# Optimization experiments

Hardware: AMD Instinct MI355X
Metric: run time of the kernel (lower is better)

## Reference

```python
import jax, jax.numpy as jnp
import numpy as np

TAIL = 3.0            # tail bound B of the unconstrained RQS
MIN_W = 1e-3
MIN_H = 1e-3
MIN_D = 1e-3
K = 8                 # number of spline bins


def conv1d(x, w, b):
    # x: [B, Cin, L], w: [Cout, Cin, k] -> [B, Cout, L] (SAME padding)
    y = jax.lax.conv_general_dilated(x, w, (1,), 'SAME',
                                     dimension_numbers=('NCH', 'OIH', 'NCH'))
    return y + b[None, :, None]


def pixelcnn(c, x, w0, b0, wh, bh, w_out, b_out):
    # conditioner: maps (c, x) -> per-channel spline params (W, H, D)
    h = jnp.concatenate([c, x], axis=1)
    h = jax.nn.relu(conv1d(h, w0, b0))
    for j in range(wh.shape[0]):
        h = jax.nn.relu(conv1d(h, wh[j], bh[j]))
    p = conv1d(h, w_out, b_out)        # [B, (3K-1)*C, L]
    p = p.mean(axis=-1)                # global pool over positions
    Bsz, C = x.shape[0], x.shape[1]
    p = p.reshape(Bsz, C, 3 * K - 1)
    return p[..., :K], p[..., K:2 * K], p[..., 2 * K:]


def _gather(p, idx):
    # p: [B, C, Kp], idx: [B, C, L] -> [B, C, L]
    return jnp.take_along_axis(p[:, :, None, :], idx[..., None], axis=-1)[..., 0]


def rqs_inverse(y, Wp, Hp, Dp):
    # Vectorized unconstrained rational-quadratic spline (inverse pass),
    # replacing the torch per-position Python loop; params broadcast over L.
    Kb = Wp.shape[-1]
    widths = MIN_W + (1 - MIN_W * Kb) * jax.nn.softmax(Wp, -1)
    cw = jnp.concatenate([jnp.zeros_like(widths[..., :1]), jnp.cumsum(widths, -1)], -1)
    cw = 2 * TAIL * cw - TAIL                      # knot x-positions [B,C,K+1]
    widths = cw[..., 1:] - cw[..., :-1]
    heights = MIN_H + (1 - MIN_H * Kb) * jax.nn.softmax(Hp, -1)
    ch = jnp.concatenate([jnp.zeros_like(heights[..., :1]), jnp.cumsum(heights, -1)], -1)
    ch = 2 * TAIL * ch - TAIL                      # knot y-positions [B,C,K+1]
    heights = ch[..., 1:] - ch[..., :-1]
    d_int = MIN_D + jax.nn.softplus(Dp)            # interior derivatives [B,C,K-1]
    ones = jnp.ones_like(d_int[..., :1])
    derivs = jnp.concatenate([ones, d_int, ones], -1)   # boundary derivs = 1

    inside = jnp.abs(y) <= TAIL                    # identity tails outside
    yc = jnp.clip(y, -TAIL, TAIL)
    # bin search over K+1 knots (broadcast compare, K is small)
    idx = jnp.clip(jnp.sum((yc[..., None] >= ch[:, :, None, :]), -1) - 1, 0, Kb - 1)

    in_cw = _gather(cw, idx); in_w = _gather(widths, idx)
    in_ch = _gather(ch, idx); in_h = _gather(heights, idx)
    dk = _gather(derivs, idx); dk1 = _gather(derivs, idx + 1)

    s = in_h / in_w
    dy = yc - in_ch
    t1 = dk + dk1 - 2 * s
    a = in_h * (s - dk) + dy * t1
    b = in_h * dk - dy * t1
    cq = -s * dy
    disc = jnp.maximum(b * b - 4 * a * cq, 0.0)
    root = (2 * cq) / (-b - jnp.sqrt(disc))        # xi in [0,1]
    out = root * in_w + in_cw
    denom = s + t1 * root * (1 - root)
    dnum = s * s * (dk1 * root * root + 2 * s * root * (1 - root) + dk * (1 - root) ** 2)
    ld = -(jnp.log(dnum) - 2 * jnp.log(denom))     # inverse logabsdet
    return jnp.where(inside, out, y), jnp.where(inside, ld, jnp.zeros_like(ld))


def flow_forward(c, noise, w0, b0, wh, bh, w_out, b_out):
    x = noise                                      # torch draws fresh N(0,1) of z.shape
    L = x.shape[-1]
    log_det = jnp.zeros((x.shape[0], 1), x.dtype)
    T = w0.shape[0]
    for t in range(T):                             # small fixed number of flow steps
        Wp, Hp, Dp = pixelcnn(c, x, w0[t], b0[t], wh[t], bh[t], w_out[t], b_out[t])
        x, ld = rqs_inverse(x, Wp, Hp, Dp)         # all L positions at once
        # torch: sum_i (sum over channels of ld_i) / L
        log_det = log_det + ld.sum(axis=(1, 2))[:, None] / L
    return x, log_det


def setup_inputs() -> dict:
    key = jax.random.key(0)
    ks = jax.random.split(key, 8)
    B, C_IN, C_OUT, L, T, HID = 128, 16, 8, 8192, 2, 32
    P = 3 * K - 1
    return {
        'z': jax.random.normal(ks[0], (B, C_OUT, L), jnp.float32),
        'c': jax.random.normal(ks[1], (B, C_IN, L), jnp.float32),
        'noise': jax.random.normal(ks[2], (B, C_OUT, L), jnp.float32),
        'w0': 0.1 * jax.random.normal(ks[3], (T, HID, C_IN + C_OUT, 3), jnp.float32),
        'b0': jnp.zeros((T, HID), jnp.float32),
        'wh': 0.1 * jax.random.normal(ks[4], (T, 3, HID, HID, 3), jnp.float32),
        'bh': jnp.zeros((T, 3, HID), jnp.float32),
        'w_out': 0.1 * jax.random.normal(ks[5], (T, P * C_OUT, HID, 1), jnp.float32),
        'b_out': jnp.zeros((T, P * C_OUT), jnp.float32),
    }


def reference(z, c, noise, w0, b0, wh, bh, w_out, b_out):
    del z  # torch forward ignores z's values; it only uses z.shape for the noise draw
    return flow_forward(c, noise, w0, b0, wh, bh, w_out, b_out)
```

## Files before the change

kernel.cpp:

```cpp
#include <hip/hip_runtime.h>
#include <hip/hip_bf16.h>

#define BATCH 128
#define CCOND 16
#define CX    8
#define CIN0  24
#define HID   32
#define LLEN  8192
#define NSTEP 2
#define PDIM  23
#define POUT  184
#define PSTR  48

#define WPW   48
#define SROWS 56
#define RSTR  40
#define LWORDS (SROWS * RSTR)
#define GRIDX 43

typedef __bf16 bf16x8 __attribute__((ext_vector_type(8)));
typedef __bf16 bf16x4 __attribute__((ext_vector_type(4)));
typedef float  f32x4  __attribute__((ext_vector_type(4)));

#define WAVE_SYNC() asm volatile("s_waitcnt lgkmcnt(0)" ::: "memory")

template<int CTRL>
__device__ __forceinline__ float dpp_movf(float v) {
    return __int_as_float(
        __builtin_amdgcn_mov_dpp(__float_as_int(v), CTRL, 0xF, 0xF, true));
}
#define RROR1 0x121
#define RROR2 0x122
#define RROR4 0x124
#define RROR8 0x128

__device__ __forceinline__ unsigned short f2bf(float f) {
    unsigned u = __float_as_uint(f);
    return (unsigned short)((u + 0x7FFFu + ((u >> 16) & 1u)) >> 16);
}

__global__ void zero_kernel(float* __restrict__ ws, float* __restrict__ logdet) {
    int i = blockIdx.x * 256 + threadIdx.x;
    ws[i] = 0.f;
    if (i < BATCH) logdet[i] = 0.f;
}

__global__ void repack_frag_kernel(const float* __restrict__ w0,
                                   const float* __restrict__ wh,
                                   unsigned short* __restrict__ wf) {
    int i = blockIdx.x * 256 + threadIdx.x;
    int j = i & 7, lane = (i >> 3) & 63, q = i >> 9;
    int mt = q & 1; q >>= 1;
    int s = q % 3;  q /= 3;
    int l = q & 3, t = q >> 2;
    int m = mt * 16 + (lane & 15);
    int ci = (lane >> 4) * 8 + j;
    float v;
    if (l == 0)
        v = (ci < CIN0) ? w0[((t * HID + m) * CIN0 + ci) * 3 + s] : 0.f;
    else
        v = wh[(((t * 3 + (l - 1)) * HID + m) * HID + ci) * 3 + s];
    wf[i] = f2bf(v);
}

template<int NTL, int LAST, bool EDGE>
__device__ __forceinline__ void wconv_layer(
        const __bf16* __restrict__ bin, __bf16* __restrict__ bout,
        const unsigned short* __restrict__ wl, const float* __restrict__ bp,
        const int (&starts)[NTL], int gb, int lane, float* __restrict__ vs) {
    const int prow = lane & 15, grp = lane >> 4;
    const int ci0 = grp * 8, co0 = grp * 4;

    bf16x8 af[3][2];
    #pragma unroll
    for (int s = 0; s < 3; ++s)
        #pragma unroll
        for (int mt = 0; mt < 2; ++mt)
            af[s][mt] = *reinterpret_cast<const bf16x8*>(
                wl + ((s * 2 + mt) << 9) + (lane << 3));
    f32x4 bias0 = *reinterpret_cast<const f32x4*>(bp + co0);
    f32x4 bias1 = *reinterpret_cast<const f32x4*>(bp + 16 + co0);

    bf16x8 bfr[NTL][3];
    #pragma unroll
    for (int t = 0; t < NTL; ++t) {
        const int o = starts[t] + prow;
        #pragma unroll
        for (int tap = 0; tap < 3; ++tap)
            bfr[t][tap] = *reinterpret_cast<const bf16x8*>(
                &bin[(o + tap - 1) * RSTR + ci0]);
    }
    __builtin_amdgcn_sched_barrier(0);

    #pragma unroll
    for (int t = 0; t < NTL; ++t) {
        const int o = starts[t] + prow;
        f32x4 a0 = bias0, a1 = bias1;
        a0 = __builtin_amdgcn_mfma_f32_16x16x32_bf16(af[0][0], bfr[t][0], a0, 0, 0, 0);
        a1 = __builtin_amdgcn_mfma_f32_16x16x32_bf16(af[0][1], bfr[t][0], a1, 0, 0, 0);
        a0 = __builtin_amdgcn_mfma_f32_16x16x32_bf16(af[1][0], bfr[t][1], a0, 0, 0, 0);
        a1 = __builtin_amdgcn_mfma_f32_16x16x32_bf16(af[1][1], bfr[t][1], a1, 0, 0, 0);
        a0 = __builtin_amdgcn_mfma_f32_16x16x32_bf16(af[2][0], bfr[t][2], a0, 0, 0, 0);
        a1 = __builtin_amdgcn_mfma_f32_16x16x32_bf16(af[2][1], bfr[t][2], a1, 0, 0, 0);
        bool ok = true;
        if (EDGE) ok = (unsigned)(gb - 4 + o) < (unsigned)LLEN;
        #pragma unroll
        for (int r = 0; r < 4; ++r) {
            a0[r] = fmaxf(a0[r], 0.f);
            a1[r] = fmaxf(a1[r], 0.f);
            if (EDGE) { a0[r] = ok ? a0[r] : 0.f; a1[r] = ok ? a1[r] : 0.f; }
        }
        if (!LAST) {
            bf16x4 p0, p1;
            #pragma unroll
            for (int r = 0; r < 4; ++r) { p0[r] = (__bf16)a0[r]; p1[r] = (__bf16)a1[r]; }
            *reinterpret_cast<bf16x4*>(&bout[o * RSTR + co0]) = p0;
            *reinterpret_cast<bf16x4*>(&bout[o * RSTR + 16 + co0]) = p1;
        } else {
            #pragma unroll
            for (int r = 0; r < 4; ++r) { vs[r] += a0[r]; vs[4 + r] += a1[r]; }
        }
    }
}

template<bool EDGE>
__device__ __forceinline__ void conv_body(
        const float* __restrict__ cin, const float* __restrict__ xin,
        const unsigned short* __restrict__ wf,
        const float* __restrict__ b0p, const float* __restrict__ bhp,
        __bf16* __restrict__ bufA, __bf16* __restrict__ bufB,
        int b, int gb, int lane, float* __restrict__ vs) {
    if (lane < SROWS) {
        const int p = lane;
        int g = gb - 4 + p;
        int gc = g;
        bool ok = true;
        if (EDGE) { gc = min(max(g, 0), LLEN - 1); ok = (g == gc); }
        const float* cbp = cin + (size_t)b * CCOND * LLEN + gc;
        const float* xbp = xin + (size_t)b * CX * LLEN + gc;
        float v[CIN0];
        #pragma unroll
        for (int ch = 0; ch < CCOND; ++ch) v[ch] = cbp[(size_t)ch * LLEN];
        #pragma unroll
        for (int ch = 0; ch < CX; ++ch) v[CCOND + ch] = xbp[(size_t)ch * LLEN];
        if (EDGE) {
            #pragma unroll
            for (int ch = 0; ch < CIN0; ++ch) v[ch] = ok ? v[ch] : 0.f;
        }
        bf16x8 pk0, pk1, pk2;
        #pragma unroll
        for (int j = 0; j < 8; ++j) {
            pk0[j] = (__bf16)v[j];
            pk1[j] = (__bf16)v[8 + j];
            pk2[j] = (__bf16)v[16 + j];
        }
        *reinterpret_cast<bf16x8*>(&bufA[p * RSTR])      = pk0;
        *reinterpret_cast<bf16x8*>(&bufA[p * RSTR + 8])  = pk1;
        *reinterpret_cast<bf16x8*>(&bufA[p * RSTR + 16]) = pk2;
        *reinterpret_cast<uint4*>(&bufA[p * RSTR + 24])  = make_uint4(0, 0, 0, 0);
    }
    WAVE_SYNC();

    const int s0[4] = {1, 17, 33, 39};
    const int s1[4] = {2, 18, 34, 38};
    const int s2[4] = {3, 19, 35, 37};
    const int s3[3] = {4, 20, 36};
    wconv_layer<4, 0, EDGE>(bufA, bufB, wf,        b0p,      s0, gb, lane, vs);
    WAVE_SYNC();
    wconv_layer<4, 0, EDGE>(bufB, bufA, wf + 3072, bhp,      s1, gb, lane, vs);
    WAVE_SYNC();
    wconv_layer<4, 0, EDGE>(bufA, bufB, wf + 6144, bhp + 32, s2, gb, lane, vs);
    WAVE_SYNC();
    wconv_layer<3, 1, EDGE>(bufB, bufA, wf + 9216, bhp + 64, s3, gb, lane, vs);
}

__global__ __launch_bounds__(256, 4) void conv_kernel(
        const float* __restrict__ cin,
        const float* __restrict__ xin,
        const unsigned short* __restrict__ wf,
        const float* __restrict__ b0p,
        const float* __restrict__ bhp,
        float* __restrict__ hbar) {
    __shared__ __align__(16) __bf16 lds[4][2][LWORDS];
    __shared__ float psum[4][HID];

    const int tid = threadIdx.x;
    const int lane = tid & 63, wv = tid >> 6;
    const int b = blockIdx.y;
    const int gb = blockIdx.x * (4 * WPW) + wv * WPW;
    const int prow = lane & 15, grp = lane >> 4;

    __bf16* bufA = &lds[wv][0][0];
    __bf16* bufB = &lds[wv][1][0];

    float vs[8] = {0.f, 0.f, 0.f, 0.f, 0.f, 0.f, 0.f, 0.f};
    const bool edge = (gb < 4) || (gb + SROWS - 4 > LLEN);
    if (edge)
        conv_body<true >(cin, xin, wf, b0p, bhp, bufA, bufB, b, gb, lane, vs);
    else
        conv_body<false>(cin, xin, wf, b0p, bhp, bufA, bufB, b, gb, lane, vs);

    #pragma unroll
    for (int r = 0; r < 8; ++r) {
        vs[r] += dpp_movf<RROR8>(vs[r]);
        vs[r] += dpp_movf<RROR4>(vs[r]);
        vs[r] += dpp_movf<RROR2>(vs[r]);
        vs[r] += dpp_movf<RROR1>(vs[r]);
    }
    const int co0 = grp * 4;
    if (prow == 0) {
        #pragma unroll
        for (int r = 0; r < 4; ++r) {
            psum[wv][co0 + r] = vs[r];
            psum[wv][16 + co0 + r] = vs[4 + r];
        }
    }
    __syncthreads();
    if (tid < HID) {
        float s = psum[0][tid] + psum[1][tid] + psum[2][tid] + psum[3][tid];
        atomicAdd(&hbar[b * HID + tid], s);
    }
}

__device__ __forceinline__ float softplusf(float v) {
    return fmaxf(v, 0.f) + log1pf(expf(-fabsf(v)));
}

__global__ __launch_bounds__(256) void params_kernel(
        const float* __restrict__ hbar,
        const float* __restrict__ w_out,
        const float* __restrict__ b_out,
        float* __restrict__ params) {
    __shared__ float wsh[POUT][HID + 1];
    __shared__ float hsh[32][HID];
    const int tid = threadIdx.x;
    const float invL = 1.0f / (float)LLEN;
    for (int i = tid; i < POUT * HID; i += 256)
        wsh[i >> 5][i & 31] = w_out[i];
    for (int i = tid; i < 32 * HID; i += 256)
        hsh[i >> 5][i & 31] = hbar[blockIdx.x * 32 * HID + i] * invL;
    __syncthreads();

    int tg = blockIdx.x * 256 + tid;
    int bl = tid >> 3, c = tid & 7;

    float p[PDIM];
    #pragma unroll
    for (int j = 0; j < PDIM; j++) {
        int cp = c * PDIM + j;
        float acc = b_out[cp];
        #pragma unroll
        for (int h = 0; h < HID; h++) acc = fmaf(wsh[cp][h], hsh[bl][h], acc);
        p[j] = acc;
    }

    float* out = params + (size_t)tg * PSTR;

    {
        float mx = p[0];
        #pragma unroll
        for (int k = 1; k < 8; k++) mx = fmaxf(mx, p[k]);
        float e[8], se = 0.f;
        #pragma unroll
        for (int k = 0; k < 8; k++) { e[k] = expf(p[k] - mx); se += e[k]; }
        float inv = 1.f / se, cum = 0.f;
        float cw[9]; cw[0] = -3.f;
        #pragma unroll
        for (int k = 0; k < 8; k++) {
            float wk = 1e-3f + (1.f - 8e-3f) * (e[k] * inv);
            cum += wk;
            cw[k + 1] = 6.f * cum - 3.f;
        }
        #pragma unroll
        for (int k = 0; k < 9; k++) out[k] = cw[k];
        #pragma unroll
        for (int k = 0; k < 8; k++) out[18 + k] = cw[k + 1] - cw[k];
    }
    {
        float mx = p[8];
        #pragma unroll
        for (int k = 1; k < 8; k++) mx = fmaxf(mx, p[8 + k]);
        float e[8], se = 0.f;
        #pragma unroll
        for (int k = 0; k < 8; k++) { e[k] = expf(p[8 + k] - mx); se += e[k]; }
        float inv = 1.f / se, cum = 0.f;
        float ch[9]; ch[0] = -3.f;
        #pragma unroll
        for (int k = 0; k < 8; k++) {
            float hk = 1e-3f + (1.f - 8e-3f) * (e[k] * inv);
            cum += hk;
            ch[k + 1] = 6.f * cum - 3.f;
        }
        #pragma unroll
        for (int k = 0; k < 9; k++) out[9 + k] = ch[k];
        #pragma unroll
        for (int k = 0; k < 8; k++) out[26 + k] = ch[k + 1] - ch[k];
    }
    out[34] = 1.f;
    #pragma unroll
    for (int k = 0; k < 7; k++) out[35 + k] = 1e-3f + softplusf(p[16 + k]);
    out[42] = 1.f;
}

__device__ __forceinline__ void rqs_elem(
        const float* cw, const float* chv, const float* wd,
        const float* hg, const float* dv,
        float y, float& ov, float& ldsum) {
    bool inside = fabsf(y) <= 3.0f;
    float yc = fminf(fmaxf(y, -3.f), 3.f);

    float icw = cw[0], iw = wd[0], ich = chv[0], ih = hg[0];
    float dk = dv[0], dk1 = dv[1];
    #pragma unroll
    for (int k = 1; k < 8; k++) {
        bool c = yc >= chv[k];
        icw = c ? cw[k]  : icw;
        iw  = c ? wd[k]  : iw;
        ich = c ? chv[k] : ich;
        ih  = c ? hg[k]  : ih;
        dk  = c ? dv[k]  : dk;
        dk1 = c ? dv[k + 1] : dk1;
    }
    float s  = ih * __builtin_amdgcn_rcpf(iw);
    float dy = yc - ich;
    float t1 = dk + dk1 - 2.f * s;
    float a  = ih * (s - dk) + dy * t1;
    float bq = ih * dk - dy * t1;
    float cq = -s * dy;
    float disc = fmaxf(bq * bq - 4.f * a * cq, 0.f);
    float den  = -bq - __builtin_amdgcn_sqrtf(disc);
    float root = (2.f * cq) * __builtin_amdgcn_rcpf(den);
    float om = 1.f - root;
    float outv  = fmaf(root, iw, icw);
    float denom = fmaf(t1 * root, om, s);
    float dnum  = s * s * (dk1 * root * root + 2.f * s * root * om + dk * om * om);
    float ld = (2.f * __builtin_amdgcn_logf(denom) - __builtin_amdgcn_logf(dnum))
               * 0.69314718055994531f;
    ov = inside ? outv : y;
    ldsum += inside ? ld : 0.f;
}

__global__ __launch_bounds__(256) void rqs_kernel(const float* __restrict__ params,
                                                  const float* __restrict__ xin,
                                                  float* __restrict__ xout,
                                                  float* __restrict__ logdet) {
    const int bc = blockIdx.y;
    const float* __restrict__ pp = params + (size_t)bc * PSTR;
    float cw[9], chv[9], wd[8], hg[8], dv[9];
    #pragma unroll
    for (int k = 0; k < 9; k++) cw[k] = pp[k];
    #pragma unroll
    for (int k = 0; k < 9; k++) chv[k] = pp[9 + k];
    #pragma unroll
    for (int k = 0; k < 8; k++) wd[k] = pp[18 + k];
    #pragma unroll
    for (int k = 0; k < 8; k++) hg[k] = pp[26 + k];
    #pragma unroll
    for (int k = 0; k < 9; k++) dv[k] = pp[34 + k];

    const int tid = threadIdx.x;
    size_t base = (size_t)bc * LLEN + (size_t)blockIdx.x * 4096 + (size_t)tid * 4;
    float4 y4[4];
    #pragma unroll
    for (int q = 0; q < 4; ++q)
        y4[q] = *reinterpret_cast<const float4*>(xin + base + q * 1024);

    float ldsum = 0.f;
    float4 o4[4];
    #pragma unroll
    for (int q = 0; q < 4; ++q) {
        rqs_elem(cw, chv, wd, hg, dv, y4[q].x, o4[q].x, ldsum);
        rqs_elem(cw, chv, wd, hg, dv, y4[q].y, o4[q].y, ldsum);
        rqs_elem(cw, chv, wd, hg, dv, y4[q].z, o4[q].z, ldsum);
        rqs_elem(cw, chv, wd, hg, dv, y4[q].w, o4[q].w, ldsum);
    }
    #pragma unroll
    for (int q = 0; q < 4; ++q)
        *reinterpret_cast<float4*>(xout + base + q * 1024) = o4[q];

    #pragma unroll
    for (int off = 32; off > 0; off >>= 1) ldsum += __shfl_xor(ldsum, off, 64);
    __shared__ float red[4];
    if ((tid & 63) == 0) red[tid >> 6] = ldsum;
    __syncthreads();
    if (tid == 0) {
        float sb = red[0] + red[1] + red[2] + red[3];
        atomicAdd(&logdet[bc >> 3], sb * (1.0f / (float)LLEN));
    }
}

extern "C" void kernel_launch(void* const* d_in, const int* in_sizes, int n_in,
                              void* d_out, int out_size, void* d_ws, size_t ws_size,
                              hipStream_t stream) {
    const float* cin   = (const float*)d_in[1];
    const float* noise = (const float*)d_in[2];
    const float* w0    = (const float*)d_in[3];
    const float* b0    = (const float*)d_in[4];
    const float* wh    = (const float*)d_in[5];
    const float* bh    = (const float*)d_in[6];
    const float* w_out = (const float*)d_in[7];
    const float* b_out = (const float*)d_in[8];

    float* xout   = (float*)d_out;
    float* logdet = xout + (size_t)BATCH * CX * LLEN;

    float* ws     = (float*)d_ws;
    float* hbar0  = ws;
    float* hbar1  = ws + 4096;
    float* params = ws + 8192;
    unsigned short* wf = (unsigned short*)(ws + 8192 + 1024 * PSTR);

    zero_kernel<<<32, 256, 0, stream>>>(ws, logdet);
    repack_frag_kernel<<<96, 256, 0, stream>>>(w0, wh, wf);

    for (int t = 0; t < NSTEP; t++) {
        const float* xcur = (t == 0) ? noise : xout;
        float* hbar = (t == 0) ? hbar0 : hbar1;
        conv_kernel<<<dim3(GRIDX, BATCH), 256, 0, stream>>>(
            cin, xcur,
            wf + t * 12288, b0 + t * HID, bh + t * 3 * HID,
            hbar);
        params_kernel<<<BATCH * CX / 256, 256, 0, stream>>>(
            hbar, w_out + t * POUT * HID, b_out + t * POUT, params);
        rqs_kernel<<<dim3(LLEN / 4096, BATCH * CX), 256, 0, stream>>>(
            params, xcur, xout, logdet);
    }
}
```

Baseline: 163.7 us.

## Convolve in place in a single LDS buffer per wave and raise occupancy

Drops the ping-pong LDS buffers and runs each conv layer in place in one buffer per wave. Every lane loads all of its input taps into registers, with a sched_barrier before any store, so overwriting the buffer is meant to be safe. This halves LDS use per block, and launch bounds go from 4 to 6 blocks per CU to turn the saved space into occupancy. Correctness depends on the staggered tile starts and within-wave ordering keeping later tiles' reads ahead of earlier tiles' writes, and the tighter launch bound may force register spills.

```diff
diff --git a/kernel.cpp b/kernel.cpp
--- a/kernel.cpp
+++ b/kernel.cpp
@@ -65,7 +65,7 @@
 
 template<int NTL, int LAST, bool EDGE>
 __device__ __forceinline__ void wconv_layer(
-        const __bf16* __restrict__ bin, __bf16* __restrict__ bout,
+        __bf16* buf,
         const unsigned short* __restrict__ wl, const float* __restrict__ bp,
         const int (&starts)[NTL], int gb, int lane, float* __restrict__ vs) {
     const int prow = lane & 15, grp = lane >> 4;
@@ -88,7 +88,7 @@
         #pragma unroll
         for (int tap = 0; tap < 3; ++tap)
             bfr[t][tap] = *reinterpret_cast<const bf16x8*>(
-                &bin[(o + tap - 1) * RSTR + ci0]);
+                &buf[(o + tap - 1) * RSTR + ci0]);
     }
     __builtin_amdgcn_sched_barrier(0);
 
@@ -114,8 +114,8 @@
             bf16x4 p0, p1;
             #pragma unroll
             for (int r = 0; r < 4; ++r) { p0[r] = (__bf16)a0[r]; p1[r] = (__bf16)a1[r]; }
-            *reinterpret_cast<bf16x4*>(&bout[o * RSTR + co0]) = p0;
-            *reinterpret_cast<bf16x4*>(&bout[o * RSTR + 16 + co0]) = p1;
+            *reinterpret_cast<bf16x4*>(&buf[o * RSTR + co0]) = p0;
+            *reinterpret_cast<bf16x4*>(&buf[o * RSTR + 16 + co0]) = p1;
         } else {
             #pragma unroll
             for (int r = 0; r < 4; ++r) { vs[r] += a0[r]; vs[4 + r] += a1[r]; }
@@ -128,7 +128,7 @@
         const float* __restrict__ cin, const float* __restrict__ xin,
         const unsigned short* __restrict__ wf,
         const float* __restrict__ b0p, const float* __restrict__ bhp,
-        __bf16* __restrict__ bufA, __bf16* __restrict__ bufB,
+        __bf16* buf,
         int b, int gb, int lane, float* __restrict__ vs) {
     if (lane < SROWS) {
         const int p = lane;
@@ -154,10 +154,10 @@
             pk1[j] = (__bf16)v[8 + j];
             pk2[j] = (__bf16)v[16 + j];
         }
-        *reinterpret_cast<bf16x8*>(&bufA[p * RSTR])      = pk0;
-        *reinterpret_cast<bf16x8*>(&bufA[p * RSTR + 8])  = pk1;
-        *reinterpret_cast<bf16x8*>(&bufA[p * RSTR + 16]) = pk2;
-        *reinterpret_cast<uint4*>(&bufA[p * RSTR + 24])  = make_uint4(0, 0, 0, 0);
+        *reinterpret_cast<bf16x8*>(&buf[p * RSTR])      = pk0;
+        *reinterpret_cast<bf16x8*>(&buf[p * RSTR + 8])  = pk1;
+        *reinterpret_cast<bf16x8*>(&buf[p * RSTR + 16]) = pk2;
+        *reinterpret_cast<uint4*>(&buf[p * RSTR + 24])  = make_uint4(0, 0, 0, 0);
     }
     WAVE_SYNC();
 
@@ -165,23 +165,23 @@
     const int s1[4] = {2, 18, 34, 38};
     const int s2[4] = {3, 19, 35, 37};
     const int s3[3] = {4, 20, 36};
-    wconv_layer<4, 0, EDGE>(bufA, bufB, wf,        b0p,      s0, gb, lane, vs);
+    wconv_layer<4, 0, EDGE>(buf, wf,        b0p,      s0, gb, lane, vs);
     WAVE_SYNC();
-    wconv_layer<4, 0, EDGE>(bufB, bufA, wf + 3072, bhp,      s1, gb, lane, vs);
+    wconv_layer<4, 0, EDGE>(buf, wf + 3072, bhp,      s1, gb, lane, vs);
     WAVE_SYNC();
-    wconv_layer<4, 0, EDGE>(bufA, bufB, wf + 6144, bhp + 32, s2, gb, lane, vs);
+    wconv_layer<4, 0, EDGE>(buf, wf + 6144, bhp + 32, s2, gb, lane, vs);
     WAVE_SYNC();
-    wconv_layer<3, 1, EDGE>(bufB, bufA, wf + 9216, bhp + 64, s3, gb, lane, vs);
-}
-
-__global__ __launch_bounds__(256, 4) void conv_kernel(
+    wconv_layer<3, 1, EDGE>(buf, wf + 9216, bhp + 64, s3, gb, lane, vs);
+}
+
+__global__ __launch_bounds__(256, 6) void conv_kernel(
         const float* __restrict__ cin,
         const float* __restrict__ xin,
         const unsigned short* __restrict__ wf,
         const float* __restrict__ b0p,
         const float* __restrict__ bhp,
         float* __restrict__ hbar) {
-    __shared__ __align__(16) __bf16 lds[4][2][LWORDS];
+    __shared__ __align__(16) __bf16 lds[4][LWORDS];
     __shared__ float psum[4][HID];
 
     const int tid = threadIdx.x;
@@ -190,15 +190,14 @@
     const int gb = blockIdx.x * (4 * WPW) + wv * WPW;
     const int prow = lane & 15, grp = lane >> 4;
 
-    __bf16* bufA = &lds[wv][0][0];
-    __bf16* bufB = &lds[wv][1][0];
+    __bf16* buf = &lds[wv][0];
 
     float vs[8] = {0.f, 0.f, 0.f, 0.f, 0.f, 0.f, 0.f, 0.f};
     const bool edge = (gb < 4) || (gb + SROWS - 4 > LLEN);
     if (edge)
-        conv_body<true >(cin, xin, wf, b0p, bhp, bufA, bufB, b, gb, lane, vs);
+        conv_body<true >(cin, xin, wf, b0p, bhp, buf, b, gb, lane, vs);
     else
-        conv_body<false>(cin, xin, wf, b0p, bhp, bufA, bufB, b, gb, lane, vs);
+        conv_body<false>(cin, xin, wf, b0p, bhp, buf, b, gb, lane, vs);
 
     #pragma unroll
     for (int r = 0; r < 8; ++r) {
```

Result: slower. 248.4 us (+51.8%).

## Fuse params computation into rqs kernel and merge init kernels

Applied to the files above, without the earlier changes.

Removes the separate params_kernel and computes the per-(batch,channel) spline parameters inside each rqs block: 23 threads do the 32-wide dot products from pooled hidden features, then three threads build the softmax knots and softplus derivatives in shared memory. The zero and weight-repack kernels are also merged into one init kernel. This drops three launches and the params workspace round trip. In exchange, each rqs block (2 per bc) redoes the small matvec and adds two barriers plus serial single-thread work before streaming.

```diff
diff --git a/kernel.cpp b/kernel.cpp
--- a/kernel.cpp
+++ b/kernel.cpp
@@ -10,7 +10,6 @@
 #define NSTEP 2
 #define PDIM  23
 #define POUT  184
-#define PSTR  48
 
 #define WPW   48
 #define SROWS 56
@@ -39,16 +38,15 @@
     return (unsigned short)((u + 0x7FFFu + ((u >> 16) & 1u)) >> 16);
 }
 
-__global__ void zero_kernel(float* __restrict__ ws, float* __restrict__ logdet) {
+__global__ void init_kernel(const float* __restrict__ w0,
+                            const float* __restrict__ wh,
+                            unsigned short* __restrict__ wf,
+                            float* __restrict__ ws,
+                            float* __restrict__ logdet) {
     int i = blockIdx.x * 256 + threadIdx.x;
-    ws[i] = 0.f;
+    if (i < 8192) ws[i] = 0.f;
     if (i < BATCH) logdet[i] = 0.f;
-}
-
-__global__ void repack_frag_kernel(const float* __restrict__ w0,
-                                   const float* __restrict__ wh,
-                                   unsigned short* __restrict__ wf) {
-    int i = blockIdx.x * 256 + threadIdx.x;
+
     int j = i & 7, lane = (i >> 3) & 63, q = i >> 9;
     int mt = q & 1; q >>= 1;
     int s = q % 3;  q /= 3;
@@ -224,82 +222,6 @@
 
 __device__ __forceinline__ float softplusf(float v) {
     return fmaxf(v, 0.f) + log1pf(expf(-fabsf(v)));
-}
-
-__global__ __launch_bounds__(256) void params_kernel(
-        const float* __restrict__ hbar,
-        const float* __restrict__ w_out,
-        const float* __restrict__ b_out,
-        float* __restrict__ params) {
-    __shared__ float wsh[POUT][HID + 1];
-    __shared__ float hsh[32][HID];
-    const int tid = threadIdx.x;
-    const float invL = 1.0f / (float)LLEN;
-    for (int i = tid; i < POUT * HID; i += 256)
-        wsh[i >> 5][i & 31] = w_out[i];
-    for (int i = tid; i < 32 * HID; i += 256)
-        hsh[i >> 5][i & 31] = hbar[blockIdx.x * 32 * HID + i] * invL;
-    __syncthreads();
-
-    int tg = blockIdx.x * 256 + tid;
-    int bl = tid >> 3, c = tid & 7;
-
-    float p[PDIM];
-    #pragma unroll
-    for (int j = 0; j < PDIM; j++) {
-        int cp = c * PDIM + j;
-        float acc = b_out[cp];
-        #pragma unroll
-        for (int h = 0; h < HID; h++) acc = fmaf(wsh[cp][h], hsh[bl][h], acc);
-        p[j] = acc;
-    }
-
-    float* out = params + (size_t)tg * PSTR;
-
-    {
-        float mx = p[0];
-        #pragma unroll
-        for (int k = 1; k < 8; k++) mx = fmaxf(mx, p[k]);
-        float e[8], se = 0.f;
-        #pragma unroll
-        for (int k = 0; k < 8; k++) { e[k] = expf(p[k] - mx); se += e[k]; }
-        float inv = 1.f / se, cum = 0.f;
-        float cw[9]; cw[0] = -3.f;
-        #pragma unroll
-        for (int k = 0; k < 8; k++) {
-            float wk = 1e-3f + (1.f - 8e-3f) * (e[k] * inv);
-            cum += wk;
-            cw[k + 1] = 6.f * cum - 3.f;
-        }
-        #pragma unroll
-        for (int k = 0; k < 9; k++) out[k] = cw[k];
-        #pragma unroll
-        for (int k = 0; k < 8; k++) out[18 + k] = cw[k + 1] - cw[k];
-    }
-    {
-        float mx = p[8];
-        #pragma unroll
-        for (int k = 1; k < 8; k++) mx = fmaxf(mx, p[8 + k]);
-        float e[8], se = 0.f;
-        #pragma unroll
-        for (int k = 0; k < 8; k++) { e[k] = expf(p[8 + k] - mx); se += e[k]; }
-        float inv = 1.f / se, cum = 0.f;
-        float ch[9]; ch[0] = -3.f;
-        #pragma unroll
-        for (int k = 0; k < 8; k++) {
-            float hk = 1e-3f + (1.f - 8e-3f) * (e[k] * inv);
-            cum += hk;
-            ch[k + 1] = 6.f * cum - 3.f;
-        }
-        #pragma unroll
-        for (int k = 0; k < 9; k++) out[9 + k] = ch[k];
-        #pragma unroll
-        for (int k = 0; k < 8; k++) out[26 + k] = ch[k + 1] - ch[k];
-    }
-    out[34] = 1.f;
-    #pragma unroll
-    for (int k = 0; k < 7; k++) out[35 + k] = 1e-3f + softplusf(p[16 + k]);
-    out[42] = 1.f;
 }
 
 __device__ __forceinline__ void rqs_elem(
@@ -340,25 +262,87 @@
     ldsum += inside ? ld : 0.f;
 }
 
-__global__ __launch_bounds__(256) void rqs_kernel(const float* __restrict__ params,
-                                                  const float* __restrict__ xin,
-                                                  float* __restrict__ xout,
-                                                  float* __restrict__ logdet) {
+__global__ __launch_bounds__(256) void rqs_kernel(
+        const float* __restrict__ hbar,
+        const float* __restrict__ w_out,
+        const float* __restrict__ b_out,
+        const float* __restrict__ xin,
+        float* __restrict__ xout,
+        float* __restrict__ logdet) {
+    __shared__ float pj[PDIM];
+    __shared__ float spl[43];
+    __shared__ float red[4];
     const int bc = blockIdx.y;
-    const float* __restrict__ pp = params + (size_t)bc * PSTR;
+    const int b = bc >> 3, c = bc & 7;
+    const int tid = threadIdx.x;
+
+    if (tid < PDIM) {
+        int cp = c * PDIM + tid;
+        float acc = b_out[cp];
+        const float* wrow = w_out + cp * HID;
+        const float* hb = hbar + b * HID;
+        const float invL = 1.0f / (float)LLEN;
+        #pragma unroll
+        for (int h = 0; h < HID; h++) acc = fmaf(wrow[h], hb[h] * invL, acc);
+        pj[tid] = acc;
+    }
+    __syncthreads();
+    if (tid == 0) {
+        float mx = pj[0];
+        #pragma unroll
+        for (int k = 1; k < 8; k++) mx = fmaxf(mx, pj[k]);
+        float e[8], se = 0.f;
+        #pragma unroll
+        for (int k = 0; k < 8; k++) { e[k] = expf(pj[k] - mx); se += e[k]; }
+        float inv = 1.f / se, cum = 0.f, prev = -3.f;
+        spl[0] = -3.f;
+        #pragma unroll
+        for (int k = 0; k < 8; k++) {
+            float wk = 1e-3f + (1.f - 8e-3f) * (e[k] * inv);
+            cum += wk;
+            float nk = 6.f * cum - 3.f;
+            spl[k + 1] = nk;
+            spl[18 + k] = nk - prev;
+            prev = nk;
+        }
+    } else if (tid == 64) {
+        float mx = pj[8];
+        #pragma unroll
+        for (int k = 1; k < 8; k++) mx = fmaxf(mx, pj[8 + k]);
+        float e[8], se = 0.f;
+        #pragma unroll
+        for (int k = 0; k < 8; k++) { e[k] = expf(pj[8 + k] - mx); se += e[k]; }
+        float inv = 1.f / se, cum = 0.f, prev = -3.f;
+        spl[9] = -3.f;
+        #pragma unroll
+        for (int k = 0; k < 8; k++) {
+            float hk = 1e-3f + (1.f - 8e-3f) * (e[k] * inv);
+            cum += hk;
+            float nk = 6.f * cum - 3.f;
+            spl[10 + k] = nk;
+            spl[26 + k] = nk - prev;
+            prev = nk;
+        }
+    } else if (tid == 128) {
+        spl[34] = 1.f;
+        #pragma unroll
+        for (int k = 0; k < 7; k++) spl[35 + k] = 1e-3f + softplusf(pj[16 + k]);
+        spl[42] = 1.f;
+    }
+    __syncthreads();
+
     float cw[9], chv[9], wd[8], hg[8], dv[9];
     #pragma unroll
-    for (int k = 0; k < 9; k++) cw[k] = pp[k];
-    #pragma unroll
-    for (int k = 0; k < 9; k++) chv[k] = pp[9 + k];
-    #pragma unroll
-    for (int k = 0; k < 8; k++) wd[k] = pp[18 + k];
-    #pragma unroll
-    for (int k = 0; k < 8; k++) hg[k] = pp[26 + k];
-    #pragma unroll
-    for (int k = 0; k < 9; k++) dv[k] = pp[34 + k];
-
-    const int tid = threadIdx.x;
+    for (int k = 0; k < 9; k++) cw[k] = spl[k];
+    #pragma unroll
+    for (int k = 0; k < 9; k++) chv[k] = spl[9 + k];
+    #pragma unroll
+    for (int k = 0; k < 8; k++) wd[k] = spl[18 + k];
+    #pragma unroll
+    for (int k = 0; k < 8; k++) hg[k] = spl[26 + k];
+    #pragma unroll
+    for (int k = 0; k < 9; k++) dv[k] = spl[34 + k];
+
     size_t base = (size_t)bc * LLEN + (size_t)blockIdx.x * 4096 + (size_t)tid * 4;
     float4 y4[4];
     #pragma unroll
@@ -380,7 +364,6 @@
 
     #pragma unroll
     for (int off = 32; off > 0; off >>= 1) ldsum += __shfl_xor(ldsum, off, 64);
-    __shared__ float red[4];
     if ((tid & 63) == 0) red[tid >> 6] = ldsum;
     __syncthreads();
     if (tid == 0) {
@@ -407,11 +390,9 @@
     float* ws     = (float*)d_ws;
     float* hbar0  = ws;
     float* hbar1  = ws + 4096;
-    float* params = ws + 8192;
-    unsigned short* wf = (unsigned short*)(ws + 8192 + 1024 * PSTR);
-
-    zero_kernel<<<32, 256, 0, stream>>>(ws, logdet);
-    repack_frag_kernel<<<96, 256, 0, stream>>>(w0, wh, wf);
+    unsigned short* wf = (unsigned short*)(ws + 8192);
+
+    init_kernel<<<96, 256, 0, stream>>>(w0, wh, wf, ws, logdet);
 
     for (int t = 0; t < NSTEP; t++) {
         const float* xcur = (t == 0) ? noise : xout;
@@ -420,9 +401,8 @@
             cin, xcur,
             wf + t * 12288, b0 + t * HID, bh + t * 3 * HID,
             hbar);
-        params_kernel<<<BATCH * CX / 256, 256, 0, stream>>>(
-            hbar, w_out + t * POUT * HID, b_out + t * POUT, params);
         rqs_kernel<<<dim3(LLEN / 4096, BATCH * CX), 256, 0, stream>>>(
-            params, xcur, xout, logdet);
-    }
-}
+            hbar, w_out + t * POUT * HID, b_out + t * POUT,
+            xcur, xout, logdet);
+    }
+}
```

Result: faster. 149.8 us (-8.5%).
